# Kernel tuning notes

Measured on AMD Instinct MI355X. Metric: run time of the kernel, lower is better.

Reference implementation:

```python
import jax, jax.numpy as jnp
import numpy as np

N = 100000      # nodes
E = 1000000     # edges (avg degree ~10)
IN_DIM = 128
OUT_DIM = 64
NEG_SLOPE = 0.2  # GATLayerST alpha


def setup_inputs() -> dict:
    key = jax.random.key(0)
    k1, k2, k3, k4, k5 = jax.random.split(key, 5)
    X = jax.random.normal(k1, (N, IN_DIM), dtype=jnp.float32)
    edge_index = jax.random.randint(k2, (2, E), 0, N, dtype=jnp.int64)
    W = jax.random.normal(k3, (IN_DIM, OUT_DIM), dtype=jnp.float32) * 0.05
    a_l = jax.random.normal(k4, (OUT_DIM,), dtype=jnp.float32) * 0.05
    a_r = jax.random.normal(k5, (OUT_DIM,), dtype=jnp.float32) * 0.05
    return {"X": X, "edge_index": edge_index, "W": W, "a_l": a_l, "a_r": a_r}


def reference(X, edge_index, W, a_l, a_r):
    # Single-head GAT (nhead=1, concat irrelevant), no residual/activation/norm,
    # dropout disabled (inference). edge_weight unused by attention path.
    src = edge_index[0]
    dst = edge_index[1]

    h = X @ W                          # [N, OUT]
    el = h @ a_l                       # [N] source-side attention term
    er = h @ a_r                       # [N] destination-side attention term

    # per-edge logits
    e = jax.nn.leaky_relu(el[src] + er[dst], negative_slope=NEG_SLOPE)  # [E]

    # segment softmax over incoming edges of each destination node
    e_max = jax.ops.segment_max(e, dst, num_segments=N)
    e_max = jnp.where(jnp.isfinite(e_max), e_max, jnp.zeros_like(e_max))
    e_exp = jnp.exp(e - e_max[dst])                                     # [E]
    denom = jax.ops.segment_sum(e_exp, dst, num_segments=N)            # [N]
    alpha = e_exp / jnp.maximum(denom[dst], 1e-16)                      # [E]

    # weighted scatter-add aggregation
    out = jax.ops.segment_sum(alpha[:, None] * h[src], dst, num_segments=N)  # [N, OUT]
    return out
```

## Files before the change

kernel.cpp:

```cpp
#include <hip/hip_runtime.h>
#include <math.h>

#define IN_DIM 128
#define OUT_DIM 64
#define NEG_SLOPE 0.2f

typedef __attribute__((ext_vector_type(8))) short short8;
typedef __attribute__((ext_vector_type(4))) float v4f;

__device__ inline unsigned short f2bf(float f) {
    unsigned u = __float_as_uint(f);
    return (unsigned short)((u + 0x7fffu + ((u >> 16) & 1u)) >> 16);
}

__global__ __launch_bounds__(256) void gemm_mfma_kernel(
        const float* __restrict__ X, const float* __restrict__ W,
        const float* __restrict__ a_l, const float* __restrict__ a_r,
        float* __restrict__ h, float* __restrict__ el, float* __restrict__ er, int n)
{
    const int tid  = threadIdx.x;
    const int lane = tid & 63;
    const int wv   = tid >> 6;
    const int r16  = lane & 15;
    const int g    = lane >> 4;

    short8 bf[4][4];
    #pragma unroll
    for (int ks = 0; ks < 4; ++ks) {
        #pragma unroll
        for (int nt = 0; nt < 4; ++nt) {
            const float* wp = W + (size_t)(ks * 32 + g * 8) * OUT_DIM + nt * 16 + r16;
            short8 b;
            #pragma unroll
            for (int j = 0; j < 8; ++j)
                b[j] = (short)f2bf(wp[(size_t)j * OUT_DIM]);
            bf[ks][nt] = b;
        }
    }

    const float alv0 = a_l[r16],      alv1 = a_l[16 + r16],
                alv2 = a_l[32 + r16], alv3 = a_l[48 + r16];
    const float arv0 = a_r[r16],      arv1 = a_r[16 + r16],
                arv2 = a_r[32 + r16], arv3 = a_r[48 + r16];

    const int wave_row0 = blockIdx.x * 256 + wv * 64;

    #pragma unroll
    for (int mt = 0; mt < 4; ++mt) {
        const int row0m = wave_row0 + mt * 16;
        if (row0m >= n) break;

        const int rowA = min(row0m + r16, n - 1);
        const float* xp = X + (size_t)rowA * IN_DIM + g * 8;

        v4f acc0 = {0.f,0.f,0.f,0.f}, acc1 = {0.f,0.f,0.f,0.f},
            acc2 = {0.f,0.f,0.f,0.f}, acc3 = {0.f,0.f,0.f,0.f};

        #pragma unroll
        for (int ks = 0; ks < 4; ++ks) {
            const float4 xa = *(const float4*)(xp + ks * 32);
            const float4 xb = *(const float4*)(xp + ks * 32 + 4);
            short8 a;
            a[0] = (short)f2bf(xa.x); a[1] = (short)f2bf(xa.y);
            a[2] = (short)f2bf(xa.z); a[3] = (short)f2bf(xa.w);
            a[4] = (short)f2bf(xb.x); a[5] = (short)f2bf(xb.y);
            a[6] = (short)f2bf(xb.z); a[7] = (short)f2bf(xb.w);
            acc0 = __builtin_amdgcn_mfma_f32_16x16x32_bf16(a, bf[ks][0], acc0, 0, 0, 0);
            acc1 = __builtin_amdgcn_mfma_f32_16x16x32_bf16(a, bf[ks][1], acc1, 0, 0, 0);
            acc2 = __builtin_amdgcn_mfma_f32_16x16x32_bf16(a, bf[ks][2], acc2, 0, 0, 0);
            acc3 = __builtin_amdgcn_mfma_f32_16x16x32_bf16(a, bf[ks][3], acc3, 0, 0, 0);
        }

        #pragma unroll
        for (int reg = 0; reg < 4; ++reg) {
            const int row = row0m + g * 4 + reg;
            if (row < n) {
                float* hp = h + (size_t)row * OUT_DIM + r16;
                hp[0]  = acc0[reg];
                hp[16] = acc1[reg];
                hp[32] = acc2[reg];
                hp[48] = acc3[reg];
            }
        }

        #pragma unroll
        for (int reg = 0; reg < 4; ++reg) {
            float t = acc0[reg]*alv0 + acc1[reg]*alv1 + acc2[reg]*alv2 + acc3[reg]*alv3;
            float u = acc0[reg]*arv0 + acc1[reg]*arv1 + acc2[reg]*arv2 + acc3[reg]*arv3;
            #pragma unroll
            for (int off = 1; off < 16; off <<= 1) {
                t += __shfl_xor(t, off);
                u += __shfl_xor(u, off);
            }
            const int row = row0m + g * 4 + reg;
            if (r16 == 0 && row < n) { el[row] = t; er[row] = u; }
        }
    }
}

__global__ void degree_rank_kernel(const int* __restrict__ dst, int* __restrict__ deg,
                                   int* __restrict__ erank, int e) {
    int i = blockIdx.x * blockDim.x + threadIdx.x;
    if (i < e) erank[i] = atomicAdd(&deg[dst[i]], 1);
}

__global__ __launch_bounds__(256) void alloc_kernel(
        const int* __restrict__ deg, int* __restrict__ cursor,
        int2* __restrict__ seg, int n)
{
    const int i    = blockIdx.x * blockDim.x + threadIdx.x;
    const int lane = threadIdx.x & 63;
    const int d    = (i < n) ? deg[i] : 0;

    int incl = d;
    #pragma unroll
    for (int off = 1; off < 64; off <<= 1) {
        int u = __shfl_up(incl, off);
        if (lane >= off) incl += u;
    }
    int base = 0;
    if (lane == 63) base = atomicAdd(cursor, incl);
    base = __shfl(base, 63);
    if (i < n) seg[i] = make_int2(base + incl - d, d);
}

__global__ void scatter_kernel(
        const int* __restrict__ src, const int* __restrict__ dst,
        const int2* __restrict__ seg, const int* __restrict__ erank,
        int* __restrict__ esrc, int e)
{
    int i = blockIdx.x * blockDim.x + threadIdx.x;
    if (i >= e) return;
    esrc[((const int*)seg)[2 * dst[i]] + erank[i]] = src[i];
}

__global__ __launch_bounds__(256) void gat_node_kernel(
        const int* __restrict__ esrc, const int2* __restrict__ seg,
        const float* __restrict__ el, const float* __restrict__ er,
        const float* __restrict__ h, float* __restrict__ out, int n)
{
    const int node = blockIdx.x * 4 + (threadIdx.x >> 6);
    const int lane = threadIdx.x & 63;
    if (node >= n) return;

    const int2 sg   = seg[node];
    const int start = sg.x;
    const int deg   = sg.y;

    float acc = 0.f;
    if (deg > 0) {
        const float erd = er[node];
        if (deg <= 64) {
            int   s = 0;
            float x = -INFINITY;
            if (lane < deg) {
                s = esrc[start + lane];
                x = el[s] + erd;
                x = (x > 0.f) ? x : NEG_SLOPE * x;
            }
            float m = x;
            #pragma unroll
            for (int off = 32; off > 0; off >>= 1) m = fmaxf(m, __shfl_xor(m, off));
            float ex = (lane < deg) ? __expf(x - m) : 0.f;
            float dsum = ex;
            #pragma unroll
            for (int off = 32; off > 0; off >>= 1) dsum += __shfl_xor(dsum, off);
            const float a = ex * (1.f / dsum);

            float acc0 = 0.f, acc1 = 0.f, acc2 = 0.f, acc3 = 0.f;
            int j = 0;
            for (; j + 4 <= deg; j += 4) {
                const float a0 = __shfl(a, j),     a1 = __shfl(a, j + 1);
                const float a2 = __shfl(a, j + 2), a3 = __shfl(a, j + 3);
                const int   s0 = __shfl(s, j),     s1 = __shfl(s, j + 1);
                const int   s2 = __shfl(s, j + 2), s3 = __shfl(s, j + 3);
                const float h0 = h[(size_t)s0 * OUT_DIM + lane];
                const float h1 = h[(size_t)s1 * OUT_DIM + lane];
                const float h2 = h[(size_t)s2 * OUT_DIM + lane];
                const float h3 = h[(size_t)s3 * OUT_DIM + lane];
                acc0 = fmaf(a0, h0, acc0);
                acc1 = fmaf(a1, h1, acc1);
                acc2 = fmaf(a2, h2, acc2);
                acc3 = fmaf(a3, h3, acc3);
            }
            for (; j < deg; ++j) {
                const float aj = __shfl(a, j);
                const int   sj = __shfl(s, j);
                acc0 = fmaf(aj, h[(size_t)sj * OUT_DIM + lane], acc0);
            }
            acc = (acc0 + acc1) + (acc2 + acc3);
        } else {
            float m = -INFINITY;
            for (int base = 0; base < deg; base += 64) {
                int idx = base + lane;
                if (idx < deg) {
                    int ss = esrc[start + idx];
                    float xx = el[ss] + erd;
                    xx = (xx > 0.f) ? xx : NEG_SLOPE * xx;
                    m = fmaxf(m, xx);
                }
            }
            #pragma unroll
            for (int off = 32; off > 0; off >>= 1) m = fmaxf(m, __shfl_xor(m, off));

            float dsum = 0.f;
            for (int base = 0; base < deg; base += 64) {
                int idx = base + lane;
                if (idx < deg) {
                    int ss = esrc[start + idx];
                    float xx = el[ss] + erd;
                    xx = (xx > 0.f) ? xx : NEG_SLOPE * xx;
                    dsum += __expf(xx - m);
                }
            }
            #pragma unroll
            for (int off = 32; off > 0; off >>= 1) dsum += __shfl_xor(dsum, off);
            const float inv = 1.f / dsum;

            float acc0 = 0.f, acc1 = 0.f, acc2 = 0.f, acc3 = 0.f;
            for (int base = 0; base < deg; base += 64) {
                int idx = base + lane;
                int   ss = 0;
                float av = 0.f;
                if (idx < deg) {
                    ss = esrc[start + idx];
                    float xx = el[ss] + erd;
                    xx = (xx > 0.f) ? xx : NEG_SLOPE * xx;
                    av = __expf(xx - m) * inv;
                }
                const int cnt = min(64, deg - base);
                int j = 0;
                for (; j + 4 <= cnt; j += 4) {
                    const float a0 = __shfl(av, j),     a1 = __shfl(av, j + 1);
                    const float a2 = __shfl(av, j + 2), a3 = __shfl(av, j + 3);
                    const int   s0 = __shfl(ss, j),     s1 = __shfl(ss, j + 1);
                    const int   s2 = __shfl(ss, j + 2), s3 = __shfl(ss, j + 3);
                    acc0 = fmaf(a0, h[(size_t)s0 * OUT_DIM + lane], acc0);
                    acc1 = fmaf(a1, h[(size_t)s1 * OUT_DIM + lane], acc1);
                    acc2 = fmaf(a2, h[(size_t)s2 * OUT_DIM + lane], acc2);
                    acc3 = fmaf(a3, h[(size_t)s3 * OUT_DIM + lane], acc3);
                }
                for (; j < cnt; ++j) {
                    const float aj = __shfl(av, j);
                    const int   sj = __shfl(ss, j);
                    acc0 = fmaf(aj, h[(size_t)sj * OUT_DIM + lane], acc0);
                }
            }
            acc = (acc0 + acc1) + (acc2 + acc3);
        }
    }
    out[(size_t)node * OUT_DIM + lane] = acc;
}

extern "C" void kernel_launch(void* const* d_in, const int* in_sizes, int n_in,
                              void* d_out, int out_size, void* d_ws, size_t ws_size,
                              hipStream_t stream) {
    const float* X   = (const float*)d_in[0];
    const int*   ei  = (const int*)  d_in[1];
    const float* W   = (const float*)d_in[2];
    const float* a_l = (const float*)d_in[3];
    const float* a_r = (const float*)d_in[4];
    float* out = (float*)d_out;

    const int n = in_sizes[0] / IN_DIM;
    const int e = in_sizes[1] / 2;
    const int* src = ei;
    const int* dst = ei + e;

    char* ws = (char*)d_ws;
    auto carve = [&](size_t bytes) {
        char* p = ws;
        ws += (bytes + 255) & ~(size_t)255;
        return p;
    };
    float* h     = (float*)carve((size_t)n * OUT_DIM * sizeof(float));
    float* el    = (float*)carve((size_t)n * sizeof(float));
    float* er    = (float*)carve((size_t)n * sizeof(float));
    int*   degc  = (int*)  carve((size_t)(n + 1) * sizeof(int));
    int2*  seg   = (int2*) carve((size_t)n * sizeof(int2));
    int*   erank = (int*)  carve((size_t)e * sizeof(int));
    int*   esrc  = (int*)  carve((size_t)e * sizeof(int));
    int*   deg    = degc;
    int*   cursor = degc + n;

    hipMemsetAsync(degc, 0, (size_t)(n + 1) * sizeof(int), stream);
    gemm_mfma_kernel<<<(n + 255) / 256, 256, 0, stream>>>(X, W, a_l, a_r, h, el, er, n);
    degree_rank_kernel<<<(e + 255) / 256, 256, 0, stream>>>(dst, deg, erank, e);
    alloc_kernel<<<(n + 255) / 256, 256, 0, stream>>>(deg, cursor, seg, n);
    scatter_kernel<<<(e + 255) / 256, 256, 0, stream>>>(src, dst, seg, erank, esrc, e);
    gat_node_kernel<<<(n + 3) / 4, 256, 0, stream>>>(esrc, seg, el, er, h, out, n);
}
```

Baseline: 255.4 us.

## Precompute edge exp weights in scatter and gather h with half-wave float2 loads

The scatter kernel now computes each edge's leaky-relu logit and its exponential, and stores (src, weight) pairs in CSR order. The node kernel then drops the max pass and the dependent el gather, and only normalises by the sum. The aggregation splits each wave into two halves that process two edges at once with float2 loads of h, then combines the halves with a shuffle. This removes the per-node el gathers and the softmax max/exp work, at the cost of a wider edge array and no max subtraction, which risks overflow for large logits.

```diff
diff --git a/kernel.cpp b/kernel.cpp
--- a/kernel.cpp
+++ b/kernel.cpp
@@ -124,132 +124,117 @@
     if (i < n) seg[i] = make_int2(base + incl - d, d);
 }
 
-__global__ void scatter_kernel(
+__global__ void scatter_w_kernel(
         const int* __restrict__ src, const int* __restrict__ dst,
+        const float* __restrict__ el, const float* __restrict__ er,
         const int2* __restrict__ seg, const int* __restrict__ erank,
-        int* __restrict__ esrc, int e)
+        int2* __restrict__ esw, int e)
 {
     int i = blockIdx.x * blockDim.x + threadIdx.x;
     if (i >= e) return;
-    esrc[((const int*)seg)[2 * dst[i]] + erank[i]] = src[i];
+    const int s = src[i], d = dst[i];
+    float x = el[s] + er[d];
+    x = (x > 0.f) ? x : NEG_SLOPE * x;
+    const float w = __expf(x);
+    const int p = ((const int*)seg)[2 * d] + erank[i];
+    esw[p] = make_int2(s, __float_as_int(w));
 }
 
 __global__ __launch_bounds__(256) void gat_node_kernel(
-        const int* __restrict__ esrc, const int2* __restrict__ seg,
-        const float* __restrict__ el, const float* __restrict__ er,
+        const int2* __restrict__ esw, const int2* __restrict__ seg,
         const float* __restrict__ h, float* __restrict__ out, int n)
 {
     const int node = blockIdx.x * 4 + (threadIdx.x >> 6);
     const int lane = threadIdx.x & 63;
+    const int half = lane >> 5;
+    const int cl   = lane & 31;
     if (node >= n) return;
 
     const int2 sg   = seg[node];
     const int start = sg.x;
     const int deg   = sg.y;
 
-    float acc = 0.f;
+    float vx = 0.f, vy = 0.f;
     if (deg > 0) {
-        const float erd = er[node];
+        float ax = 0.f, ay = 0.f, bx = 0.f, by = 0.f;
         if (deg <= 64) {
-            int   s = 0;
-            float x = -INFINITY;
+            int s = 0; float w = 0.f;
             if (lane < deg) {
-                s = esrc[start + lane];
-                x = el[s] + erd;
-                x = (x > 0.f) ? x : NEG_SLOPE * x;
-            }
-            float m = x;
-            #pragma unroll
-            for (int off = 32; off > 0; off >>= 1) m = fmaxf(m, __shfl_xor(m, off));
-            float ex = (lane < deg) ? __expf(x - m) : 0.f;
-            float dsum = ex;
+                const int2 p = esw[start + lane];
+                s = p.x; w = __int_as_float(p.y);
+            }
+            float dsum = w;
             #pragma unroll
             for (int off = 32; off > 0; off >>= 1) dsum += __shfl_xor(dsum, off);
-            const float a = ex * (1.f / dsum);
-
-            float acc0 = 0.f, acc1 = 0.f, acc2 = 0.f, acc3 = 0.f;
-            int j = 0;
-            for (; j + 4 <= deg; j += 4) {
-                const float a0 = __shfl(a, j),     a1 = __shfl(a, j + 1);
-                const float a2 = __shfl(a, j + 2), a3 = __shfl(a, j + 3);
-                const int   s0 = __shfl(s, j),     s1 = __shfl(s, j + 1);
-                const int   s2 = __shfl(s, j + 2), s3 = __shfl(s, j + 3);
-                const float h0 = h[(size_t)s0 * OUT_DIM + lane];
-                const float h1 = h[(size_t)s1 * OUT_DIM + lane];
-                const float h2 = h[(size_t)s2 * OUT_DIM + lane];
-                const float h3 = h[(size_t)s3 * OUT_DIM + lane];
-                acc0 = fmaf(a0, h0, acc0);
-                acc1 = fmaf(a1, h1, acc1);
-                acc2 = fmaf(a2, h2, acc2);
-                acc3 = fmaf(a3, h3, acc3);
-            }
-            for (; j < deg; ++j) {
-                const float aj = __shfl(a, j);
-                const int   sj = __shfl(s, j);
-                acc0 = fmaf(aj, h[(size_t)sj * OUT_DIM + lane], acc0);
-            }
-            acc = (acc0 + acc1) + (acc2 + acc3);
+            const float alpha = w * (1.f / dsum);
+
+            int j0 = 0;
+            for (; j0 + 4 <= deg; j0 += 4) {
+                const int   ja = j0 + half,         jb = j0 + 2 + half;
+                const float aa = __shfl(alpha, ja), ab = __shfl(alpha, jb);
+                const int   sa = __shfl(s, ja),     sb = __shfl(s, jb);
+                const float2 ha = *(const float2*)(h + (size_t)sa * OUT_DIM + 2 * cl);
+                const float2 hb = *(const float2*)(h + (size_t)sb * OUT_DIM + 2 * cl);
+                ax = fmaf(aa, ha.x, ax); ay = fmaf(aa, ha.y, ay);
+                bx = fmaf(ab, hb.x, bx); by = fmaf(ab, hb.y, by);
+            }
+            for (; j0 < deg; j0 += 2) {
+                const int j = j0 + half;
+                if (j < deg) {
+                    const float aj = __shfl(alpha, j);
+                    const int   sj = __shfl(s, j);
+                    const float2 hj = *(const float2*)(h + (size_t)sj * OUT_DIM + 2 * cl);
+                    ax = fmaf(aj, hj.x, ax); ay = fmaf(aj, hj.y, ay);
+                }
+            }
         } else {
-            float m = -INFINITY;
-            for (int base = 0; base < deg; base += 64) {
-                int idx = base + lane;
-                if (idx < deg) {
-                    int ss = esrc[start + idx];
-                    float xx = el[ss] + erd;
-                    xx = (xx > 0.f) ? xx : NEG_SLOPE * xx;
-                    m = fmaxf(m, xx);
-                }
-            }
-            #pragma unroll
-            for (int off = 32; off > 0; off >>= 1) m = fmaxf(m, __shfl_xor(m, off));
-
             float dsum = 0.f;
             for (int base = 0; base < deg; base += 64) {
-                int idx = base + lane;
-                if (idx < deg) {
-                    int ss = esrc[start + idx];
-                    float xx = el[ss] + erd;
-                    xx = (xx > 0.f) ? xx : NEG_SLOPE * xx;
-                    dsum += __expf(xx - m);
-                }
+                const int idx = base + lane;
+                if (idx < deg) dsum += __int_as_float(esw[start + idx].y);
             }
             #pragma unroll
             for (int off = 32; off > 0; off >>= 1) dsum += __shfl_xor(dsum, off);
             const float inv = 1.f / dsum;
 
-            float acc0 = 0.f, acc1 = 0.f, acc2 = 0.f, acc3 = 0.f;
             for (int base = 0; base < deg; base += 64) {
-                int idx = base + lane;
-                int   ss = 0;
-                float av = 0.f;
+                const int idx = base + lane;
+                const int cnt = min(64, deg - base);
+                int s = 0; float w = 0.f;
                 if (idx < deg) {
-                    ss = esrc[start + idx];
-                    float xx = el[ss] + erd;
-                    xx = (xx > 0.f) ? xx : NEG_SLOPE * xx;
-                    av = __expf(xx - m) * inv;
-                }
-                const int cnt = min(64, deg - base);
-                int j = 0;
-                for (; j + 4 <= cnt; j += 4) {
-                    const float a0 = __shfl(av, j),     a1 = __shfl(av, j + 1);
-                    const float a2 = __shfl(av, j + 2), a3 = __shfl(av, j + 3);
-                    const int   s0 = __shfl(ss, j),     s1 = __shfl(ss, j + 1);
-                    const int   s2 = __shfl(ss, j + 2), s3 = __shfl(ss, j + 3);
-                    acc0 = fmaf(a0, h[(size_t)s0 * OUT_DIM + lane], acc0);
-                    acc1 = fmaf(a1, h[(size_t)s1 * OUT_DIM + lane], acc1);
-                    acc2 = fmaf(a2, h[(size_t)s2 * OUT_DIM + lane], acc2);
-                    acc3 = fmaf(a3, h[(size_t)s3 * OUT_DIM + lane], acc3);
-                }
-                for (; j < cnt; ++j) {
-                    const float aj = __shfl(av, j);
-                    const int   sj = __shfl(ss, j);
-                    acc0 = fmaf(aj, h[(size_t)sj * OUT_DIM + lane], acc0);
-                }
-            }
-            acc = (acc0 + acc1) + (acc2 + acc3);
-        }
-    }
-    out[(size_t)node * OUT_DIM + lane] = acc;
+                    const int2 p = esw[start + idx];
+                    s = p.x; w = __int_as_float(p.y);
+                }
+                const float alpha = w * inv;
+                int j0 = 0;
+                for (; j0 + 4 <= cnt; j0 += 4) {
+                    const int   ja = j0 + half,         jb = j0 + 2 + half;
+                    const float aa = __shfl(alpha, ja), ab = __shfl(alpha, jb);
+                    const int   sa = __shfl(s, ja),     sb = __shfl(s, jb);
+                    const float2 ha = *(const float2*)(h + (size_t)sa * OUT_DIM + 2 * cl);
+                    const float2 hb = *(const float2*)(h + (size_t)sb * OUT_DIM + 2 * cl);
+                    ax = fmaf(aa, ha.x, ax); ay = fmaf(aa, ha.y, ay);
+                    bx = fmaf(ab, hb.x, bx); by = fmaf(ab, hb.y, by);
+                }
+                for (; j0 < cnt; j0 += 2) {
+                    const int j = j0 + half;
+                    if (j < cnt) {
+                        const float aj = __shfl(alpha, j);
+                        const int   sj = __shfl(s, j);
+                        const float2 hj = *(const float2*)(h + (size_t)sj * OUT_DIM + 2 * cl);
+                        ax = fmaf(aj, hj.x, ax); ay = fmaf(aj, hj.y, ay);
+                    }
+                }
+            }
+        }
+        vx = ax + bx; vy = ay + by;
+        vx += __shfl_xor(vx, 32);
+        vy += __shfl_xor(vy, 32);
+    }
+    if (half == 0) {
+        float2 o; o.x = vx; o.y = vy;
+        *(float2*)(out + (size_t)node * OUT_DIM + 2 * cl) = o;
+    }
 }
 
 extern "C" void kernel_launch(void* const* d_in, const int* in_sizes, int n_in,
@@ -279,7 +264,7 @@
     int*   degc  = (int*)  carve((size_t)(n + 1) * sizeof(int));
     int2*  seg   = (int2*) carve((size_t)n * sizeof(int2));
     int*   erank = (int*)  carve((size_t)e * sizeof(int));
-    int*   esrc  = (int*)  carve((size_t)e * sizeof(int));
+    int2*  esw   = (int2*) carve((size_t)e * sizeof(int2));
     int*   deg    = degc;
     int*   cursor = degc + n;
 
@@ -287,6 +272,6 @@
     gemm_mfma_kernel<<<(n + 255) / 256, 256, 0, stream>>>(X, W, a_l, a_r, h, el, er, n);
     degree_rank_kernel<<<(e + 255) / 256, 256, 0, stream>>>(dst, deg, erank, e);
     alloc_kernel<<<(n + 255) / 256, 256, 0, stream>>>(deg, cursor, seg, n);
-    scatter_kernel<<<(e + 255) / 256, 256, 0, stream>>>(src, dst, seg, erank, esrc, e);
-    gat_node_kernel<<<(n + 3) / 4, 256, 0, stream>>>(esrc, seg, el, er, h, out, n);
-}
+    scatter_w_kernel<<<(e + 255) / 256, 256, 0, stream>>>(src, dst, el, er, seg, erank, esw, e);
+    gat_node_kernel<<<(n + 3) / 4, 256, 0, stream>>>(esw, seg, h, out, n);
+}
```

Measured after the change: 242.8 us. -4.9%, faster.
